# Kernel optimization log

Measured on AMD Instinct MI355X. Metric: run time of the kernel, lower is better.

The kernel has to match this reference:

```python
import jax, jax.numpy as jnp
import numpy as np

B, S, E, H = 2, 2048, 1024, 16
DH = E // H


def setup_inputs() -> dict:
    key = jax.random.key(0)
    ks = jax.random.split(key, 9)
    inp = {
        "query": jax.random.normal(ks[0], (B, S, E), dtype=jnp.float32),
        "key": jax.random.normal(ks[1], (B, S, E), dtype=jnp.float32),
        "value": jax.random.normal(ks[2], (B, S, E), dtype=jnp.float32),
        # causal mask: True means "masked out" (masked_fill semantics)
        "mask": jnp.broadcast_to(
            jnp.triu(jnp.ones((S, S), dtype=bool), k=1)[None, None], (B, 1, S, S)
        ),
        # learned parameters (nn.Linear weight is [out, in]; y = x @ W.T + b)
        "Wq": jax.random.normal(ks[3], (E, E), dtype=jnp.float32) / np.sqrt(E),
        "Wk": jax.random.normal(ks[4], (E, E), dtype=jnp.float32) / np.sqrt(E),
        "Wv": jax.random.normal(ks[5], (E, E), dtype=jnp.float32) / np.sqrt(E),
        "Wo": jax.random.normal(ks[6], (E, E), dtype=jnp.float32) / np.sqrt(E),
        "bo": jax.random.normal(ks[7], (E,), dtype=jnp.float32) * 0.01,
    }
    return inp


def reference(query, key, value, mask, Wq, Wk, Wv, Wo, bo):
    # projections (no bias for q/k/v)
    Q = query @ Wq.T  # [B,S,E]
    K = key @ Wk.T
    V = value @ Wv.T
    # split heads: [B,S,E] -> [B,H,S,Dh]
    Q = Q.reshape(B, S, H, DH).transpose(0, 2, 1, 3)
    K = K.reshape(B, S, H, DH).transpose(0, 2, 1, 3)
    V = V.reshape(B, S, H, DH).transpose(0, 2, 1, 3)
    scale = 1.0 / np.sqrt(DH).astype(np.float32)
    scores = jnp.einsum("bhqd,bhkd->bhqk", Q, K) * scale  # [B,H,S,S]
    scores = jnp.where(mask, -jnp.inf, scores)
    attn = jax.nn.softmax(scores, axis=-1)
    # dropout(p=0.2) is identity in eval mode
    out = jnp.einsum("bhqk,bhkd->bhqd", attn, V)  # [B,H,S,Dh]
    out = out.transpose(0, 2, 1, 3).reshape(B, S, E)
    return out @ Wo.T + bo
```

## Files before the change

### kernel.cpp

```cpp
#include <hip/hip_runtime.h>
#include <hip/hip_bf16.h>
#include <stdint.h>

#define Bb 2
#define Ss 2048
#define Ee 1024
#define Hh 16
#define Dh 64

typedef __bf16 bf16_t;
typedef __attribute__((ext_vector_type(8))) __bf16 bf16x8;
typedef __attribute__((ext_vector_type(4))) __bf16 bf16x4;
typedef __attribute__((ext_vector_type(4))) float f32x4;

#define QSCALE_LOG2E 0.18033688011112042f

__device__ inline void gload_lds16(const void* g, void* l) {
  __builtin_amdgcn_global_load_lds((__attribute__((address_space(1))) void*)g,
                                   (__attribute__((address_space(3))) void*)l,
                                   16, 0, 0);
}

__device__ inline void wg_barrier() {
  asm volatile("s_barrier" ::: "memory");
}

__device__ __forceinline__ int p_addr64(int q, int kv) {
  return q * 128 + ((((kv >> 3) ^ q) & 7) << 4) + (kv & 7) * 2;
}

struct Cvt7 {
  const float* s[7];
  bf16_t* d[7];
  int n8[7];
};

__global__ __launch_bounds__(256) void cvt_f32_bf16(Cvt7 c) {
  int gid = blockIdx.x * 256 + threadIdx.x;
#pragma unroll
  for (int j = 0; j < 7; ++j) {
    if (gid < c.n8[j]) {
      const float* s = c.s[j] + (size_t)gid * 8;
      const f32x4 lo = *(const f32x4*)s;
      const f32x4 hi = *(const f32x4*)(s + 4);
      bf16x8 v;
      v[0] = (bf16_t)lo[0]; v[1] = (bf16_t)lo[1];
      v[2] = (bf16_t)lo[2]; v[3] = (bf16_t)lo[3];
      v[4] = (bf16_t)hi[0]; v[5] = (bf16_t)hi[1];
      v[6] = (bf16_t)hi[2]; v[7] = (bf16_t)hi[3];
      *(bf16x8*)(c.d[j] + (size_t)gid * 8) = v;
      return;
    }
    gid -= c.n8[j];
  }
}

template <int ROWS>
__device__ __forceinline__ void stage_bf16(const bf16_t* __restrict__ src,
                                           int ldk, int k0, bf16_t* lds,
                                           int wave, int lane) {
  const int srow = lane >> 3, sslot = lane & 7;
#pragma unroll
  for (int r = 0; r < ROWS / 32; ++r) {
    const int chunk = wave + r * 4;
    const int row = chunk * 8 + srow;
    const int k16 = sslot ^ (row & 7);
    gload_lds16(src + (size_t)row * ldk + k0 + k16 * 8, lds + chunk * 512);
  }
}

__device__ __forceinline__ void mfma_tile_128(const bf16_t* As,
                                              const bf16_t* Bs, int wr, int wc,
                                              int lr, int lg, f32x4 acc[4][4]) {
  const char* a_base = (const char*)As;
  const char* b_base = (const char*)Bs;
#pragma unroll
  for (int kk = 0; kk < 2; ++kk) {
    bf16x8 af[4], bfr[4];
#pragma unroll
    for (int x = 0; x < 4; ++x) {
      const int arow = wr * 64 + x * 16 + lr;
      af[x] = *(const bf16x8*)(a_base + ((arow * 128 + kk * 64 + lg * 16) ^
                                         ((arow & 7) << 4)));
      const int brow = wc * 64 + x * 16 + lr;
      bfr[x] = *(const bf16x8*)(b_base + ((brow * 128 + kk * 64 + lg * 16) ^
                                          ((brow & 7) << 4)));
    }
#pragma unroll
    for (int mi = 0; mi < 4; ++mi)
#pragma unroll
      for (int ni = 0; ni < 4; ++ni)
        acc[mi][ni] = __builtin_amdgcn_mfma_f32_16x16x32_bf16(
            af[mi], bfr[ni], acc[mi][ni], 0, 0, 0);
  }
}

__global__ __launch_bounds__(256) void qkv_proj(
    const bf16_t* __restrict__ Aq, const bf16_t* __restrict__ Ak,
    const bf16_t* __restrict__ Av, const bf16_t* __restrict__ Wq,
    const bf16_t* __restrict__ Wk, const bf16_t* __restrict__ Wv,
    bf16_t* __restrict__ Cq, bf16_t* __restrict__ Ck,
    bf16_t* __restrict__ Cv) {
  __shared__ bf16_t As[2][128 * 64];
  __shared__ bf16_t Bs[2][128 * 64];
  const int z = blockIdx.z;
  const bf16_t* A = (z == 0) ? Aq : (z == 1) ? Ak : Av;
  const bf16_t* W = (z == 0) ? Wq : (z == 1) ? Wk : Wv;
  bf16_t* C = (z == 0) ? Cq : (z == 1) ? Ck : Cv;

  const int wg = blockIdx.y * 8 + blockIdx.x;
  const int virt = (wg & 7) * 32 + (wg >> 3);
  const int n0 = (virt & 7) * 128, m0 = (virt >> 3) * 128;

  const int tid = threadIdx.x;
  const int lane = tid & 63, wave = tid >> 6;
  const int wr = wave >> 1, wc = wave & 1;
  const int lr = lane & 15, lg = lane >> 4;

  const bf16_t* Arow = A + (size_t)m0 * Ee;
  const bf16_t* Wrow = W + (size_t)n0 * Ee;

  f32x4 acc[4][4] = {};

  stage_bf16<128>(Arow, Ee, 0, As[0], wave, lane);
  stage_bf16<128>(Wrow, Ee, 0, Bs[0], wave, lane);
  stage_bf16<128>(Arow, Ee, 64, As[1], wave, lane);
  stage_bf16<128>(Wrow, Ee, 64, Bs[1], wave, lane);

  for (int t = 0; t < 16; ++t) {
    const int cur = t & 1;
    if (t < 15)
      asm volatile("s_waitcnt vmcnt(8)" ::: "memory");
    else
      asm volatile("s_waitcnt vmcnt(0)" ::: "memory");
    wg_barrier();
    mfma_tile_128(As[cur], Bs[cur], wr, wc, lr, lg, acc);
    wg_barrier();
    if (t + 2 < 16) {
      stage_bf16<128>(Arow, Ee, (t + 2) * 64, As[cur], wave, lane);
      stage_bf16<128>(Wrow, Ee, (t + 2) * 64, Bs[cur], wave, lane);
    }
  }

#pragma unroll
  for (int mi = 0; mi < 4; ++mi) {
#pragma unroll
    for (int i = 0; i < 4; ++i) {
      const int m = m0 + wr * 64 + mi * 16 + lg * 4 + i;
#pragma unroll
      for (int ni = 0; ni < 4; ++ni) {
        const int n = n0 + wc * 64 + ni * 16 + lr;
        float v = acc[mi][ni][i];
        if (z == 0) v *= QSCALE_LOG2E;
        const int b = m >> 11, s = m & (Ss - 1);
        const int h = n >> 6, d = n & 63;
        if (z != 2)
          C[(((size_t)(b * Hh + h)) * Ss + s) * Dh + d] = (bf16_t)v;
        else
          C[(((size_t)(b * Hh + h)) * Dh + d) * Ss + s] = (bf16_t)v;
      }
    }
  }
}

__global__ __launch_bounds__(256) void out_gemm(const bf16_t* __restrict__ A,
                                                const bf16_t* __restrict__ W,
                                                const float* __restrict__ bias,
                                                float* __restrict__ C) {
  __shared__ bf16_t As[2][128 * 64];
  __shared__ bf16_t Bs[2][64 * 64];
  const int wg = blockIdx.y * 16 + blockIdx.x;
  const int virt = (wg & 7) * 64 + (wg >> 3);
  const int n0 = (virt & 15) * 64, m0 = (virt >> 4) * 128;

  const int tid = threadIdx.x;
  const int lane = tid & 63, wave = tid >> 6;
  const int lr = lane & 15, lg = lane >> 4;

  const bf16_t* Arow = A + (size_t)m0 * Ee;
  const bf16_t* Wrow = W + (size_t)n0 * Ee;

  f32x4 acc[2][4] = {};

  stage_bf16<128>(Arow, Ee, 0, As[0], wave, lane);
  stage_bf16<64>(Wrow, Ee, 0, Bs[0], wave, lane);
  stage_bf16<128>(Arow, Ee, 64, As[1], wave, lane);
  stage_bf16<64>(Wrow, Ee, 64, Bs[1], wave, lane);

  for (int t = 0; t < 16; ++t) {
    const int cur = t & 1;
    if (t < 15)
      asm volatile("s_waitcnt vmcnt(6)" ::: "memory");
    else
      asm volatile("s_waitcnt vmcnt(0)" ::: "memory");
    wg_barrier();

    const char* a_base = (const char*)As[cur];
    const char* b_base = (const char*)Bs[cur];
#pragma unroll
    for (int kk = 0; kk < 2; ++kk) {
      bf16x8 af[2], bfr[4];
#pragma unroll
      for (int x = 0; x < 2; ++x) {
        const int arow = wave * 32 + x * 16 + lr;
        af[x] = *(const bf16x8*)(a_base + ((arow * 128 + kk * 64 + lg * 16) ^
                                           ((arow & 7) << 4)));
      }
#pragma unroll
      for (int ni = 0; ni < 4; ++ni) {
        const int brow = ni * 16 + lr;
        bfr[ni] = *(const bf16x8*)(b_base + ((brow * 128 + kk * 64 + lg * 16) ^
                                             ((brow & 7) << 4)));
      }
#pragma unroll
      for (int mi = 0; mi < 2; ++mi)
#pragma unroll
        for (int ni = 0; ni < 4; ++ni)
          acc[mi][ni] = __builtin_amdgcn_mfma_f32_16x16x32_bf16(
              af[mi], bfr[ni], acc[mi][ni], 0, 0, 0);
    }
    wg_barrier();
    if (t + 2 < 16) {
      stage_bf16<128>(Arow, Ee, (t + 2) * 64, As[cur], wave, lane);
      stage_bf16<64>(Wrow, Ee, (t + 2) * 64, Bs[cur], wave, lane);
    }
  }

#pragma unroll
  for (int mi = 0; mi < 2; ++mi) {
#pragma unroll
    for (int i = 0; i < 4; ++i) {
      const int m = m0 + wave * 32 + mi * 16 + lg * 4 + i;
#pragma unroll
      for (int ni = 0; ni < 4; ++ni) {
        const int n = n0 + ni * 16 + lr;
        C[(size_t)m * Ee + n] = acc[mi][ni][i] + bias[n];
      }
    }
  }
}


__device__ __forceinline__ void attn_stage(const bf16_t* Kh, const bf16_t* Vh,
                                           int kv0, int wave, int lane,
                                           bf16_t* KsBuf, bf16_t* VsBuf) {
#pragma unroll
  for (int r = 0; r < 2; ++r) {
    const int c = wave + r * 4;
    const int row = c * 8 + (lane >> 3);
    const int sl = (lane & 7) ^ (row & 7);
    gload_lds16(Kh + (size_t)(kv0 + row) * Dh + sl * 8, KsBuf + c * 512);
    gload_lds16(Vh + (size_t)row * Ss + kv0 + sl * 8, VsBuf + c * 512);
  }
}

template <bool MASKED>
__device__ __forceinline__ void attn_tile_compute(
    int kv0, int qw, int lane, char* pb, const char* kb, const char* vb,
    const bf16x8 aq[2], float& m_run, float& l_run, f32x4 oacc[4]) {
  const int lr = lane & 15, lg = lane >> 4;

  f32x4 sc[4];
#pragma unroll
  for (int ni = 0; ni < 4; ++ni) {
    const int krow = ni * 16 + lr;
    const bf16x8 ak0 =
        *(const bf16x8*)(kb + ((krow * 128 + lg * 16) ^ ((krow & 7) << 4)));
    const bf16x8 ak1 = *(const bf16x8*)(kb + ((krow * 128 + 64 + lg * 16) ^
                                              ((krow & 7) << 4)));
    f32x4 z = {0.f, 0.f, 0.f, 0.f};
    z = __builtin_amdgcn_mfma_f32_16x16x32_bf16(ak0, aq[0], z, 0, 0, 0);
    z = __builtin_amdgcn_mfma_f32_16x16x32_bf16(ak1, aq[1], z, 0, 0, 0);
    sc[ni] = z;
  }

  if (MASKED) {
    const int q_rel = qw + lr - kv0;
#pragma unroll
    for (int ni = 0; ni < 4; ++ni)
#pragma unroll
      for (int i = 0; i < 4; ++i)
        if (ni * 16 + lg * 4 + i > q_rel) sc[ni][i] = -1e30f;
  }

  f32x4 vm = sc[0];
#pragma unroll
  for (int ni = 1; ni < 4; ++ni)
#pragma unroll
    for (int i = 0; i < 4; ++i) vm[i] = fmaxf(vm[i], sc[ni][i]);
  float rm = fmaxf(fmaxf(vm[0], vm[1]), fmaxf(vm[2], vm[3]));
  rm = fmaxf(rm, __shfl_xor(rm, 16));
  rm = fmaxf(rm, __shfl_xor(rm, 32));

  const float mo = m_run;
  const float mn = fmaxf(mo, rm);
  const float corr = __builtin_amdgcn_exp2f(mo - mn);
  m_run = mn;

  f32x4 vs = {0.f, 0.f, 0.f, 0.f};
#pragma unroll
  for (int ni = 0; ni < 4; ++ni) {
    bf16x4 w;
#pragma unroll
    for (int i = 0; i < 4; ++i) {
      const float p = __builtin_amdgcn_exp2f(sc[ni][i] - mn);
      vs[i] += p;
      w[i] = (bf16_t)p;
    }
    *(bf16x4*)(pb + p_addr64(lr, ni * 16 + lg * 4)) = w;
  }
  float rs = (vs[0] + vs[1]) + (vs[2] + vs[3]);
  rs += __shfl_xor(rs, 16);
  rs += __shfl_xor(rs, 32);
  l_run = l_run * corr + rs;

#pragma unroll
  for (int i = 0; i < 4; ++i) {
    const float ci = __shfl(corr, (lane & 48) | (lg * 4 + i));
#pragma unroll
    for (int di = 0; di < 4; ++di) oacc[di][i] *= ci;
  }

#pragma unroll
  for (int kk = 0; kk < 2; ++kk) {
    const bf16x8 pa = *(const bf16x8*)(pb + p_addr64(lr, kk * 32 + lg * 8));
#pragma unroll
    for (int di = 0; di < 4; ++di) {
      const int vrow = di * 16 + lr;
      const bf16x8 bv = *(const bf16x8*)(vb + ((vrow * 128 + kk * 64 +
                                                lg * 16) ^
                                               ((vrow & 7) << 4)));
      oacc[di] =
          __builtin_amdgcn_mfma_f32_16x16x32_bf16(pa, bv, oacc[di], 0, 0, 0);
    }
  }
}

__device__ __forceinline__ void flash_qtile(int qt, const bf16_t* Qh,
                                            const bf16_t* Kh, const bf16_t* Vh,
                                            bf16_t* AO_row, int wave, int lane,
                                            bf16_t* Ks, bf16_t* Vs,
                                            bf16_t* PsW) {
  const int lr = lane & 15, lg = lane >> 4;
  const int qw = qt * 64 + wave * 16;

  bf16x8 aq[2];
#pragma unroll
  for (int kd = 0; kd < 2; ++kd)
    aq[kd] = *(const bf16x8*)(Qh + (size_t)(qw + lr) * Dh + kd * 32 + lg * 8);

  f32x4 oacc[4] = {};
  float m_run = -1e30f, l_run = 0.f;
  char* pb = (char*)PsW;

  const int nt = qt + 1;
  attn_stage(Kh, Vh, 0, wave, lane, Ks, Vs);

  for (int t = 0; t < nt; ++t) {
    const int cur = t & 1;
    if (t + 1 < nt) {
      attn_stage(Kh, Vh, (t + 1) * 64, wave, lane, Ks + (cur ^ 1) * 4096,
                 Vs + (cur ^ 1) * 4096);
      asm volatile("s_waitcnt vmcnt(4)" ::: "memory");
    } else {
      asm volatile("s_waitcnt vmcnt(0)" ::: "memory");
    }
    wg_barrier();
    const char* kb = (const char*)(Ks + cur * 4096);
    const char* vb = (const char*)(Vs + cur * 4096);
    if (t < nt - 1)
      attn_tile_compute<false>(t * 64, qw, lane, pb, kb, vb, aq, m_run, l_run,
                               oacc);
    else
      attn_tile_compute<true>(t * 64, qw, lane, pb, kb, vb, aq, m_run, l_run,
                              oacc);
    wg_barrier();
  }

#pragma unroll
  for (int i = 0; i < 4; ++i) {
    const float li = __shfl(l_run, (lane & 48) | (lg * 4 + i));
    const float inv = 1.0f / li;
    const int s = qw + lg * 4 + i;
#pragma unroll
    for (int di = 0; di < 4; ++di) {
      const int d = di * 16 + lr;
      AO_row[(size_t)s * Ee + d] = (bf16_t)(oacc[di][i] * inv);
    }
  }
}

__global__ __launch_bounds__(256, 4) void attn_causal(
    const bf16_t* __restrict__ Qg, const bf16_t* __restrict__ Kg,
    const bf16_t* __restrict__ Vg, bf16_t* __restrict__ AO) {
  const int wg = blockIdx.y * 16 + blockIdx.x;
  const int virt = (wg & 7) * 64 + (wg >> 3);
  const int qx = virt & 15;
  const int bh = virt >> 4;

  const int tid = threadIdx.x;
  const int lane = tid & 63, wave = tid >> 6;

  const bf16_t* Qh = Qg + (size_t)bh * Ss * Dh;
  const bf16_t* Kh = Kg + (size_t)bh * Ss * Dh;
  const bf16_t* Vh = Vg + (size_t)bh * Dh * Ss;
  const int b = bh >> 4, h = bh & 15;
  bf16_t* AO_row = AO + (size_t)b * Ss * Ee + h * 64;

  __shared__ bf16_t Ks[2][64 * 64];
  __shared__ bf16_t Vs[2][64 * 64];
  __shared__ bf16_t Ps[4][16 * 64];

  const int qtA = qx;
  const int qtB = 31 - qx;
  flash_qtile(qtA, Qh, Kh, Vh, AO_row, wave, lane, Ks[0], Vs[0], Ps[wave]);
  flash_qtile(qtB, Qh, Kh, Vh, AO_row, wave, lane, Ks[0], Vs[0], Ps[wave]);
}

extern "C" void kernel_launch(void* const* d_in, const int* in_sizes, int n_in,
                              void* d_out, int out_size, void* d_ws,
                              size_t ws_size, hipStream_t stream) {
  const float* query = (const float*)d_in[0];
  const float* key = (const float*)d_in[1];
  const float* value = (const float*)d_in[2];
  const float* Wq = (const float*)d_in[4];
  const float* Wk = (const float*)d_in[5];
  const float* Wv = (const float*)d_in[6];
  const float* Wo = (const float*)d_in[7];
  const float* bo = (const float*)d_in[8];

  const size_t T = (size_t)Bb * Ss * Ee;
  const size_t WN = (size_t)Ee * Ee;
  bf16_t* qbf = (bf16_t*)d_ws;
  bf16_t* kbf = qbf + T;
  bf16_t* vbf = kbf + T;
  bf16_t* wqb = vbf + T;
  bf16_t* wkb = wqb + WN;
  bf16_t* wvb = wkb + WN;
  bf16_t* wob = wvb + WN;
  bf16_t* qws = wob + WN;
  bf16_t* kws = qws + T;
  bf16_t* vws = kws + T;
  bf16_t* aows = qbf;

  Cvt7 c;
  c.s[0] = query; c.d[0] = qbf; c.n8[0] = (int)(T / 8);
  c.s[1] = key;   c.d[1] = kbf; c.n8[1] = (int)(T / 8);
  c.s[2] = value; c.d[2] = vbf; c.n8[2] = (int)(T / 8);
  c.s[3] = Wq;    c.d[3] = wqb; c.n8[3] = (int)(WN / 8);
  c.s[4] = Wk;    c.d[4] = wkb; c.n8[4] = (int)(WN / 8);
  c.s[5] = Wv;    c.d[5] = wvb; c.n8[5] = (int)(WN / 8);
  c.s[6] = Wo;    c.d[6] = wob; c.n8[6] = (int)(WN / 8);
  const int total8 = (int)((3 * T + 4 * WN) / 8);

  dim3 blk(256);
  cvt_f32_bf16<<<dim3(total8 / 256), blk, 0, stream>>>(c);
  qkv_proj<<<dim3(Ee / 128, (Bb * Ss) / 128, 3), blk, 0, stream>>>(
      qbf, kbf, vbf, wqb, wkb, wvb, qws, kws, vws);
  attn_causal<<<dim3(16, Bb * Hh), blk, 0, stream>>>(qws, kws, vws, aows);
  out_gemm<<<dim3(Ee / 64, (Bb * Ss) / 128), blk, 0, stream>>>(
      aows, wob, bo, (float*)d_out);
}
```

Baseline: 125.6 us.

## Shrink QKV tiles to 128x64 and split causal attention into one q-tile per block

```diff
diff --git a/kernel.cpp b/kernel.cpp
--- a/kernel.cpp
+++ b/kernel.cpp
@@ -69,30 +69,67 @@
   }
 }
 
-__device__ __forceinline__ void mfma_tile_128(const bf16_t* As,
-                                              const bf16_t* Bs, int wr, int wc,
-                                              int lr, int lg, f32x4 acc[4][4]) {
-  const char* a_base = (const char*)As;
-  const char* b_base = (const char*)Bs;
-#pragma unroll
-  for (int kk = 0; kk < 2; ++kk) {
-    bf16x8 af[4], bfr[4];
-#pragma unroll
-    for (int x = 0; x < 4; ++x) {
-      const int arow = wr * 64 + x * 16 + lr;
-      af[x] = *(const bf16x8*)(a_base + ((arow * 128 + kk * 64 + lg * 16) ^
-                                         ((arow & 7) << 4)));
-      const int brow = wc * 64 + x * 16 + lr;
-      bfr[x] = *(const bf16x8*)(b_base + ((brow * 128 + kk * 64 + lg * 16) ^
-                                          ((brow & 7) << 4)));
-    }
-#pragma unroll
-    for (int mi = 0; mi < 4; ++mi)
+template <typename EPI>
+__device__ __forceinline__ void gemm_128x64(const bf16_t* Arow,
+                                            const bf16_t* Wrow, bf16_t* As,
+                                            bf16_t* Bs, int wave, int lane,
+                                            EPI epi) {
+  const int lr = lane & 15, lg = lane >> 4;
+  f32x4 acc[2][4] = {};
+
+  stage_bf16<128>(Arow, Ee, 0, As, wave, lane);
+  stage_bf16<64>(Wrow, Ee, 0, Bs, wave, lane);
+  stage_bf16<128>(Arow, Ee, 64, As + 8192, wave, lane);
+  stage_bf16<64>(Wrow, Ee, 64, Bs + 4096, wave, lane);
+
+  for (int t = 0; t < 16; ++t) {
+    const int cur = t & 1;
+    if (t < 15)
+      asm volatile("s_waitcnt vmcnt(6)" ::: "memory");
+    else
+      asm volatile("s_waitcnt vmcnt(0)" ::: "memory");
+    wg_barrier();
+
+    const char* a_base = (const char*)(As + cur * 8192);
+    const char* b_base = (const char*)(Bs + cur * 4096);
+#pragma unroll
+    for (int kk = 0; kk < 2; ++kk) {
+      bf16x8 af[2], bfr[4];
+#pragma unroll
+      for (int x = 0; x < 2; ++x) {
+        const int arow = wave * 32 + x * 16 + lr;
+        af[x] = *(const bf16x8*)(a_base + ((arow * 128 + kk * 64 + lg * 16) ^
+                                           ((arow & 7) << 4)));
+      }
+#pragma unroll
+      for (int ni = 0; ni < 4; ++ni) {
+        const int brow = ni * 16 + lr;
+        bfr[ni] = *(const bf16x8*)(b_base + ((brow * 128 + kk * 64 + lg * 16) ^
+                                             ((brow & 7) << 4)));
+      }
+#pragma unroll
+      for (int mi = 0; mi < 2; ++mi)
+#pragma unroll
+        for (int ni = 0; ni < 4; ++ni)
+          acc[mi][ni] = __builtin_amdgcn_mfma_f32_16x16x32_bf16(
+              af[mi], bfr[ni], acc[mi][ni], 0, 0, 0);
+    }
+    wg_barrier();
+    if (t + 2 < 16) {
+      stage_bf16<128>(Arow, Ee, (t + 2) * 64, As + cur * 8192, wave, lane);
+      stage_bf16<64>(Wrow, Ee, (t + 2) * 64, Bs + cur * 4096, wave, lane);
+    }
+  }
+
+#pragma unroll
+  for (int mi = 0; mi < 2; ++mi)
+#pragma unroll
+    for (int i = 0; i < 4; ++i) {
+      const int mloc = wave * 32 + mi * 16 + lg * 4 + i;
 #pragma unroll
       for (int ni = 0; ni < 4; ++ni)
-        acc[mi][ni] = __builtin_amdgcn_mfma_f32_16x16x32_bf16(
-            af[mi], bfr[ni], acc[mi][ni], 0, 0, 0);
-  }
+        epi(mloc, ni * 16 + lr, acc[mi][ni][i]);
+    }
 }
 
 __global__ __launch_bounds__(256) void qkv_proj(
@@ -102,65 +139,29 @@
     bf16_t* __restrict__ Cq, bf16_t* __restrict__ Ck,
     bf16_t* __restrict__ Cv) {
   __shared__ bf16_t As[2][128 * 64];
-  __shared__ bf16_t Bs[2][128 * 64];
+  __shared__ bf16_t Bs[2][64 * 64];
   const int z = blockIdx.z;
   const bf16_t* A = (z == 0) ? Aq : (z == 1) ? Ak : Av;
   const bf16_t* W = (z == 0) ? Wq : (z == 1) ? Wk : Wv;
   bf16_t* C = (z == 0) ? Cq : (z == 1) ? Ck : Cv;
 
-  const int wg = blockIdx.y * 8 + blockIdx.x;
-  const int virt = (wg & 7) * 32 + (wg >> 3);
-  const int n0 = (virt & 7) * 128, m0 = (virt >> 3) * 128;
-
-  const int tid = threadIdx.x;
-  const int lane = tid & 63, wave = tid >> 6;
-  const int wr = wave >> 1, wc = wave & 1;
-  const int lr = lane & 15, lg = lane >> 4;
-
-  const bf16_t* Arow = A + (size_t)m0 * Ee;
-  const bf16_t* Wrow = W + (size_t)n0 * Ee;
-
-  f32x4 acc[4][4] = {};
-
-  stage_bf16<128>(Arow, Ee, 0, As[0], wave, lane);
-  stage_bf16<128>(Wrow, Ee, 0, Bs[0], wave, lane);
-  stage_bf16<128>(Arow, Ee, 64, As[1], wave, lane);
-  stage_bf16<128>(Wrow, Ee, 64, Bs[1], wave, lane);
-
-  for (int t = 0; t < 16; ++t) {
-    const int cur = t & 1;
-    if (t < 15)
-      asm volatile("s_waitcnt vmcnt(8)" ::: "memory");
-    else
-      asm volatile("s_waitcnt vmcnt(0)" ::: "memory");
-    wg_barrier();
-    mfma_tile_128(As[cur], Bs[cur], wr, wc, lr, lg, acc);
-    wg_barrier();
-    if (t + 2 < 16) {
-      stage_bf16<128>(Arow, Ee, (t + 2) * 64, As[cur], wave, lane);
-      stage_bf16<128>(Wrow, Ee, (t + 2) * 64, Bs[cur], wave, lane);
-    }
-  }
-
-#pragma unroll
-  for (int mi = 0; mi < 4; ++mi) {
-#pragma unroll
-    for (int i = 0; i < 4; ++i) {
-      const int m = m0 + wr * 64 + mi * 16 + lg * 4 + i;
-#pragma unroll
-      for (int ni = 0; ni < 4; ++ni) {
-        const int n = n0 + wc * 64 + ni * 16 + lr;
-        float v = acc[mi][ni][i];
-        if (z == 0) v *= QSCALE_LOG2E;
-        const int b = m >> 11, s = m & (Ss - 1);
-        const int h = n >> 6, d = n & 63;
-        if (z != 2)
-          C[(((size_t)(b * Hh + h)) * Ss + s) * Dh + d] = (bf16_t)v;
-        else
-          C[(((size_t)(b * Hh + h)) * Dh + d) * Ss + s] = (bf16_t)v;
-      }
-    }
-  }
+  const int wg = blockIdx.y * 16 + blockIdx.x;
+  const int virt = (wg & 7) * 64 + (wg >> 3);
+  const int n0 = (virt & 15) * 64, m0 = (virt >> 4) * 128;
+
+  const int lane = threadIdx.x & 63, wave = threadIdx.x >> 6;
+
+  gemm_128x64(A + (size_t)m0 * Ee, W + (size_t)n0 * Ee, As[0], Bs[0], wave,
+              lane, [&](int mloc, int nloc, float v) {
+                const int m = m0 + mloc, n = n0 + nloc;
+                if (z == 0) v *= QSCALE_LOG2E;
+                const int b = m >> 11, s = m & (Ss - 1);
+                const int h = n >> 6, d = n & 63;
+                if (z != 2)
+                  C[(((size_t)(b * Hh + h)) * Ss + s) * Dh + d] = (bf16_t)v;
+                else
+                  C[(((size_t)(b * Hh + h)) * Dh + d) * Ss + s] = (bf16_t)v;
+              });
 }
 
 __global__ __launch_bounds__(256) void out_gemm(const bf16_t* __restrict__ A,
@@ -173,71 +174,13 @@
   const int virt = (wg & 7) * 64 + (wg >> 3);
   const int n0 = (virt & 15) * 64, m0 = (virt >> 4) * 128;
 
-  const int tid = threadIdx.x;
-  const int lane = tid & 63, wave = tid >> 6;
-  const int lr = lane & 15, lg = lane >> 4;
-
-  const bf16_t* Arow = A + (size_t)m0 * Ee;
-  const bf16_t* Wrow = W + (size_t)n0 * Ee;
-
-  f32x4 acc[2][4] = {};
-
-  stage_bf16<128>(Arow, Ee, 0, As[0], wave, lane);
-  stage_bf16<64>(Wrow, Ee, 0, Bs[0], wave, lane);
-  stage_bf16<128>(Arow, Ee, 64, As[1], wave, lane);
-  stage_bf16<64>(Wrow, Ee, 64, Bs[1], wave, lane);
-
-  for (int t = 0; t < 16; ++t) {
-    const int cur = t & 1;
-    if (t < 15)
-      asm volatile("s_waitcnt vmcnt(6)" ::: "memory");
-    else
-      asm volatile("s_waitcnt vmcnt(0)" ::: "memory");
-    wg_barrier();
-
-    const char* a_base = (const char*)As[cur];
-    const char* b_base = (const char*)Bs[cur];
-#pragma unroll
-    for (int kk = 0; kk < 2; ++kk) {
-      bf16x8 af[2], bfr[4];
-#pragma unroll
-      for (int x = 0; x < 2; ++x) {
-        const int arow = wave * 32 + x * 16 + lr;
-        af[x] = *(const bf16x8*)(a_base + ((arow * 128 + kk * 64 + lg * 16) ^
-                                           ((arow & 7) << 4)));
-      }
-#pragma unroll
-      for (int ni = 0; ni < 4; ++ni) {
-        const int brow = ni * 16 + lr;
-        bfr[ni] = *(const bf16x8*)(b_base + ((brow * 128 + kk * 64 + lg * 16) ^
-                                             ((brow & 7) << 4)));
-      }
-#pragma unroll
-      for (int mi = 0; mi < 2; ++mi)
-#pragma unroll
-        for (int ni = 0; ni < 4; ++ni)
-          acc[mi][ni] = __builtin_amdgcn_mfma_f32_16x16x32_bf16(
-              af[mi], bfr[ni], acc[mi][ni], 0, 0, 0);
-    }
-    wg_barrier();
-    if (t + 2 < 16) {
-      stage_bf16<128>(Arow, Ee, (t + 2) * 64, As[cur], wave, lane);
-      stage_bf16<64>(Wrow, Ee, (t + 2) * 64, Bs[cur], wave, lane);
-    }
-  }
-
-#pragma unroll
-  for (int mi = 0; mi < 2; ++mi) {
-#pragma unroll
-    for (int i = 0; i < 4; ++i) {
-      const int m = m0 + wave * 32 + mi * 16 + lg * 4 + i;
-#pragma unroll
-      for (int ni = 0; ni < 4; ++ni) {
-        const int n = n0 + ni * 16 + lr;
-        C[(size_t)m * Ee + n] = acc[mi][ni][i] + bias[n];
-      }
-    }
-  }
+  const int lane = threadIdx.x & 63, wave = threadIdx.x >> 6;
+
+  gemm_128x64(A + (size_t)m0 * Ee, W + (size_t)n0 * Ee, As[0], Bs[0], wave,
+              lane, [&](int mloc, int nloc, float v) {
+                const int n = n0 + nloc;
+                C[(size_t)(m0 + mloc) * Ee + n] = v + bias[n];
+              });
 }
 
 
@@ -336,12 +279,29 @@
   }
 }
 
-__device__ __forceinline__ void flash_qtile(int qt, const bf16_t* Qh,
-                                            const bf16_t* Kh, const bf16_t* Vh,
-                                            bf16_t* AO_row, int wave, int lane,
-                                            bf16_t* Ks, bf16_t* Vs,
-                                            bf16_t* PsW) {
+__global__ __launch_bounds__(256, 4) void attn_causal(
+    const bf16_t* __restrict__ Qg, const bf16_t* __restrict__ Kg,
+    const bf16_t* __restrict__ Vg, bf16_t* __restrict__ AO) {
+  const int wg = blockIdx.y * 32 + blockIdx.x;
+  const int virt = (wg & 7) * 128 + (wg >> 3);
+  const int bh = virt >> 5;
+  const int i_ = virt & 31;
+  const int qt = (i_ & 1) ? 31 - (i_ >> 1) : (i_ >> 1);
+
+  const int tid = threadIdx.x;
+  const int lane = tid & 63, wave = tid >> 6;
   const int lr = lane & 15, lg = lane >> 4;
+
+  const bf16_t* Qh = Qg + (size_t)bh * Ss * Dh;
+  const bf16_t* Kh = Kg + (size_t)bh * Ss * Dh;
+  const bf16_t* Vh = Vg + (size_t)bh * Dh * Ss;
+  const int b = bh >> 4, h = bh & 15;
+  bf16_t* AO_row = AO + (size_t)b * Ss * Ee + h * 64;
+
+  __shared__ bf16_t Ks[2][64 * 64];
+  __shared__ bf16_t Vs[2][64 * 64];
+  __shared__ bf16_t Ps[4][16 * 64];
+
   const int qw = qt * 64 + wave * 16;
 
   bf16x8 aq[2];
@@ -351,23 +311,22 @@
 
   f32x4 oacc[4] = {};
   float m_run = -1e30f, l_run = 0.f;
-  char* pb = (char*)PsW;
+  char* pb = (char*)Ps[wave];
 
   const int nt = qt + 1;
-  attn_stage(Kh, Vh, 0, wave, lane, Ks, Vs);
+  attn_stage(Kh, Vh, 0, wave, lane, Ks[0], Vs[0]);
 
   for (int t = 0; t < nt; ++t) {
     const int cur = t & 1;
     if (t + 1 < nt) {
-      attn_stage(Kh, Vh, (t + 1) * 64, wave, lane, Ks + (cur ^ 1) * 4096,
-                 Vs + (cur ^ 1) * 4096);
+      attn_stage(Kh, Vh, (t + 1) * 64, wave, lane, Ks[cur ^ 1], Vs[cur ^ 1]);
       asm volatile("s_waitcnt vmcnt(4)" ::: "memory");
     } else {
       asm volatile("s_waitcnt vmcnt(0)" ::: "memory");
     }
     wg_barrier();
-    const char* kb = (const char*)(Ks + cur * 4096);
-    const char* vb = (const char*)(Vs + cur * 4096);
+    const char* kb = (const char*)Ks[cur];
+    const char* vb = (const char*)Vs[cur];
     if (t < nt - 1)
       attn_tile_compute<false>(t * 64, qw, lane, pb, kb, vb, aq, m_run, l_run,
                                oacc);
@@ -388,33 +347,6 @@
       AO_row[(size_t)s * Ee + d] = (bf16_t)(oacc[di][i] * inv);
     }
   }
-}
-
-__global__ __launch_bounds__(256, 4) void attn_causal(
-    const bf16_t* __restrict__ Qg, const bf16_t* __restrict__ Kg,
-    const bf16_t* __restrict__ Vg, bf16_t* __restrict__ AO) {
-  const int wg = blockIdx.y * 16 + blockIdx.x;
-  const int virt = (wg & 7) * 64 + (wg >> 3);
-  const int qx = virt & 15;
-  const int bh = virt >> 4;
-
-  const int tid = threadIdx.x;
-  const int lane = tid & 63, wave = tid >> 6;
-
-  const bf16_t* Qh = Qg + (size_t)bh * Ss * Dh;
-  const bf16_t* Kh = Kg + (size_t)bh * Ss * Dh;
-  const bf16_t* Vh = Vg + (size_t)bh * Dh * Ss;
-  const int b = bh >> 4, h = bh & 15;
-  bf16_t* AO_row = AO + (size_t)b * Ss * Ee + h * 64;
-
-  __shared__ bf16_t Ks[2][64 * 64];
-  __shared__ bf16_t Vs[2][64 * 64];
-  __shared__ bf16_t Ps[4][16 * 64];
-
-  const int qtA = qx;
-  const int qtB = 31 - qx;
-  flash_qtile(qtA, Qh, Kh, Vh, AO_row, wave, lane, Ks[0], Vs[0], Ps[wave]);
-  flash_qtile(qtB, Qh, Kh, Vh, AO_row, wave, lane, Ks[0], Vs[0], Ps[wave]);
 }
 
 extern "C" void kernel_launch(void* const* d_in, const int* in_sizes, int n_in,
@@ -455,9 +387,9 @@
 
   dim3 blk(256);
   cvt_f32_bf16<<<dim3(total8 / 256), blk, 0, stream>>>(c);
-  qkv_proj<<<dim3(Ee / 128, (Bb * Ss) / 128, 3), blk, 0, stream>>>(
+  qkv_proj<<<dim3(Ee / 64, (Bb * Ss) / 128, 3), blk, 0, stream>>>(
       qbf, kbf, vbf, wqb, wkb, wvb, qws, kws, vws);
-  attn_causal<<<dim3(16, Bb * Hh), blk, 0, stream>>>(qws, kws, vws, aows);
+  attn_causal<<<dim3(32, Bb * Hh), blk, 0, stream>>>(qws, kws, vws, aows);
   out_gemm<<<dim3(Ee / 64, (Bb * Ss) / 128), blk, 0, stream>>>(
       aows, wob, bo, (float*)d_out);
 }
```

New measurement: 140.1 us. 11.5% more time.
